# Optimization experiments

Measured on AMD Instinct MI355X. Metric: run time of the kernel, lower is better.

The kernel has to match this reference:

```python
import jax, jax.numpy as jnp
import numpy as np

EPS = 1e-05


def _project_to_poincare_ball(v, eps=EPS):
    # scale = clamp((1-eps)/(||v||+1e-10), max=1.0)
    norm = jnp.sqrt(jnp.sum(v * v, axis=-1, keepdims=True))
    scale = jnp.minimum((1.0 - eps) / (norm + 1e-10), 1.0)
    return v * scale


def setup_inputs() -> dict:
    key = jax.random.key(0)
    k1, k2 = jax.random.split(key)
    B, S, D, V = 2, 2048, 1024, 32000
    hidden_states = jax.random.normal(k1, (B, S, D), dtype=jnp.float32)
    weight = jax.random.normal(k2, (V, D), dtype=jnp.float32)
    return {"hidden_states": hidden_states, "weight": weight}


def reference(hidden_states, weight):
    eps = EPS
    B, S, D = hidden_states.shape
    x = _project_to_poincare_ball(hidden_states.reshape(-1, D), eps)  # (N, D)
    y = _project_to_poincare_ball(weight, eps)                        # (V, D)

    x_sq = jnp.sum(x * x, axis=-1)  # (N,)
    y_sq = jnp.sum(y * y, axis=-1)  # (V,)

    # NOTE: the original feeds this (non-squared) distance into the Poincare
    # formula (variable misnamed diff_norm_sq); we reproduce that exactly.
    d2 = x_sq[:, None] + y_sq[None, :] - 2.0 * jnp.einsum('nd,vd->nv', x, y)
    dist_euclid = jnp.sqrt(jnp.maximum(d2, 0.0))  # (N, V)

    denom = (1.0 - x_sq)[:, None] * (1.0 - y_sq)[None, :]  # (N, V)
    argument = 1.0 + 2.0 * dist_euclid / (denom + eps)
    argument = jnp.maximum(argument, 1.0 + eps)
    distances = jnp.arccosh(argument)  # (N, V)

    logits = -distances
    return logits.reshape(B, S, -1)
```

## Files before the change

kernel.cpp:

```cpp
#include <hip/hip_runtime.h>
#include <math.h>
#include <stdint.h>

#define EPS 1e-5f

typedef __bf16 bf16x8 __attribute__((ext_vector_type(8)));
typedef __bf16 bf16x4 __attribute__((ext_vector_type(4)));
typedef float  f32x4  __attribute__((ext_vector_type(4)));

constexpr int D  = 1024;
constexpr int BM = 128;
constexpr int BN = 128;

__global__ __launch_bounds__(256) void project_convert_kernel(
    const float* __restrict__ src, __bf16* __restrict__ dst,
    float* __restrict__ q_out)
{
    const int row = blockIdx.x;
    const int t = threadIdx.x;
    const float4 v = *(const float4*)(src + (size_t)row * D + t * 4);
    float s = v.x * v.x + v.y * v.y + v.z * v.z + v.w * v.w;
#pragma unroll
    for (int off = 32; off > 0; off >>= 1) s += __shfl_down(s, off);
    __shared__ float partial[4];
    __shared__ float s_scale;
    if ((t & 63) == 0) partial[t >> 6] = s;
    __syncthreads();
    if (t == 0) {
        float tot = partial[0] + partial[1] + partial[2] + partial[3];
        float norm = sqrtf(tot);
        float sc = fminf((1.0f - EPS) / (norm + 1e-10f), 1.0f);
        s_scale = sc;
        q_out[row] = sc * sc * tot;
    }
    __syncthreads();
    const float sc = s_scale;
    bf16x4 o = { (__bf16)(v.x * sc), (__bf16)(v.y * sc),
                 (__bf16)(v.z * sc), (__bf16)(v.w * sc) };
    *(bf16x4*)(dst + (size_t)row * D + t * 4) = o;
}

__device__ __forceinline__ void gload16(const void* g, void* l)
{
    __builtin_amdgcn_global_load_lds(
        (const __attribute__((address_space(1))) uint32_t*)g,
        (__attribute__((address_space(3))) uint32_t*)l, 16, 0, 0);
}

__global__ __launch_bounds__(256, 3) void hyp_gemm_bf16_kernel(
    const __bf16* __restrict__ Xb, const __bf16* __restrict__ Yb,
    const float* __restrict__ xq, const float* __restrict__ yq,
    float* __restrict__ out, int V, int nbx)
{
    constexpr int BK   = 64;
    constexpr int KT   = D / BK;
    constexpr int ROWB = BK * 2;

    __shared__ __bf16 As[BM * BK];
    __shared__ __bf16 Bs[BN * BK];

    const int wg = blockIdx.x;
    const int c = (gridDim.x & 7) ? wg : ((wg & 7) * (gridDim.x >> 3) + (wg >> 3));
    const int m0 = (c / nbx) * BM;
    const int n0 = (c % nbx) * BN;

    const int t = threadIdx.x;

    const int rt = t >> 3;
    const int gsrc = (t & 7) ^ (rt & 7);
    const char* xg = (const char*)(Xb + (size_t)(m0 + rt) * D) + gsrc * 16;
    const char* yg = (const char*)(Yb + (size_t)(n0 + rt) * D) + gsrc * 16;
    char* la = (char*)As + t * 16;
    char* lb = (char*)Bs + t * 16;

    const int lane = t & 63;
    const int ln   = lane & 15;
    const int quad = lane >> 4;
    const int wave = t >> 6;
    const int wm = (wave & 1) * 64;
    const int wn = (wave >> 1) * 64;
    const int swz = ln & 7;

    f32x4 acc[4][4] = {};

#pragma unroll
    for (int kt = 0; kt < KT; ++kt) {
        __syncthreads();
        const int ko = kt * 128;
#pragma unroll
        for (int j = 0; j < 4; ++j) {
            gload16(xg + j * 65536 + ko, la + j * 4096);
            gload16(yg + j * 65536 + ko, lb + j * 4096);
        }
        __syncthreads();
#pragma unroll
        for (int ks = 0; ks < 2; ++ks) {
            bf16x8 af[4], bfr[4];
#pragma unroll
            for (int i = 0; i < 4; ++i) {
                const int ga = ((ks * 4 + quad) ^ swz) * 16;
                af[i]  = *(const bf16x8*)((const char*)As + (wm + i * 16 + ln) * ROWB + ga);
                bfr[i] = *(const bf16x8*)((const char*)Bs + (wn + i * 16 + ln) * ROWB + ga);
            }
#pragma unroll
            for (int mt = 0; mt < 4; ++mt)
#pragma unroll
                for (int nt = 0; nt < 4; ++nt)
                    acc[mt][nt] = __builtin_amdgcn_mfma_f32_16x16x32_bf16(
                        af[mt], bfr[nt], acc[mt][nt], 0, 0, 0);
        }
    }

    float yqv[4], omy[4];
    int gcv[4];
#pragma unroll
    for (int nt = 0; nt < 4; ++nt) {
        const int gc = n0 + wn + nt * 16 + ln;
        gcv[nt] = gc;
        yqv[nt] = yq[gc];
        omy[nt] = 1.0f - yqv[nt];
    }
#pragma unroll
    for (int mt = 0; mt < 4; ++mt) {
#pragma unroll
        for (int r = 0; r < 4; ++r) {
            const int gm = m0 + wm + mt * 16 + quad * 4 + r;
            const float xqv = xq[gm];
            const float omx = 1.0f - xqv;
            float* orow = out + (size_t)gm * V;
#pragma unroll
            for (int nt = 0; nt < 4; ++nt) {
                const float dot = acc[mt][nt][r];
                float d2 = fmaxf(xqv + yqv[nt] - 2.0f * dot, 0.0f);
                float d  = __builtin_amdgcn_sqrtf(d2);
                float denom = omx * omy[nt] + EPS;
                float w = d * __builtin_amdgcn_rcpf(denom);
                float res;
                if (__builtin_expect(w >= 4.0f, 1)) {
                    res = __logf(2.0f + 4.0f * w);
                } else {
                    float arg = fmaxf(1.0f + 2.0f * w, 1.0f + EPS);
                    res = __logf(arg + __builtin_amdgcn_sqrtf(arg * arg - 1.0f));
                }
                orow[gcv[nt]] = -res;
            }
        }
    }
}

constexpr int LDT = 40;

__global__ __launch_bounds__(256) void row_stats_kernel(
    const float* __restrict__ src, float* __restrict__ scale_out,
    float* __restrict__ sq_out)
{
    const int row = blockIdx.x;
    const int t = threadIdx.x;
    const float4 v = *(const float4*)(src + (size_t)row * D + t * 4);
    float s = v.x * v.x + v.y * v.y + v.z * v.z + v.w * v.w;
#pragma unroll
    for (int off = 32; off > 0; off >>= 1) s += __shfl_down(s, off);
    __shared__ float partial[4];
    if ((t & 63) == 0) partial[t >> 6] = s;
    __syncthreads();
    if (t == 0) {
        float tot = partial[0] + partial[1] + partial[2] + partial[3];
        float norm = sqrtf(tot);
        float sc = fminf((1.0f - EPS) / (norm + 1e-10f), 1.0f);
        scale_out[row] = sc;
        sq_out[row] = sc * sc * tot;
    }
}

__global__ __launch_bounds__(256) void hyp_gemm_kernel(
    const float* __restrict__ X, const float* __restrict__ Y,
    const float* __restrict__ sx, const float* __restrict__ xq,
    const float* __restrict__ sy, const float* __restrict__ yq,
    float* __restrict__ out, int V)
{
    constexpr int BK = 32;
    __shared__ __bf16 As[BM * LDT];
    __shared__ __bf16 Bs[BN * LDT];

    const int t  = threadIdx.x;
    const int m0 = blockIdx.y * BM;
    const int n0 = blockIdx.x * BN;

    const int sr = t >> 3;
    const int scol = t & 7;

    const float* xg = X + (size_t)(m0 + sr) * D + scol * 4;
    const float* yg = Y + (size_t)(n0 + sr) * D + scol * 4;

    const int lane = t & 63;
    const int wave = t >> 6;
    const int wm = (wave & 1) * 64;
    const int wn = (wave >> 1) * 64;
    const int ln = lane & 15;
    const int quad = lane >> 4;

    f32x4 acc[4][4] = {};

    float4 pa[4], pb[4];
#pragma unroll
    for (int j = 0; j < 4; ++j) {
        pa[j] = *(const float4*)(xg + (size_t)j * 32 * D);
        pb[j] = *(const float4*)(yg + (size_t)j * 32 * D);
    }

    constexpr int KT = D / BK;
    for (int kt = 0; kt < KT; ++kt) {
        __syncthreads();
#pragma unroll
        for (int j = 0; j < 4; ++j) {
            bf16x4 a4 = { (__bf16)pa[j].x, (__bf16)pa[j].y, (__bf16)pa[j].z, (__bf16)pa[j].w };
            bf16x4 b4 = { (__bf16)pb[j].x, (__bf16)pb[j].y, (__bf16)pb[j].z, (__bf16)pb[j].w };
            *(bf16x4*)&As[(sr + 32 * j) * LDT + scol * 4] = a4;
            *(bf16x4*)&Bs[(sr + 32 * j) * LDT + scol * 4] = b4;
        }
        __syncthreads();
        if (kt + 1 < KT) {
            const int koff = (kt + 1) * BK;
#pragma unroll
            for (int j = 0; j < 4; ++j) {
                pa[j] = *(const float4*)(xg + (size_t)j * 32 * D + koff);
                pb[j] = *(const float4*)(yg + (size_t)j * 32 * D + koff);
            }
        }
        bf16x8 af[4], bfr[4];
#pragma unroll
        for (int i = 0; i < 4; ++i) {
            af[i]  = *(const bf16x8*)&As[(wm + i * 16 + ln) * LDT + quad * 8];
            bfr[i] = *(const bf16x8*)&Bs[(wn + i * 16 + ln) * LDT + quad * 8];
        }
#pragma unroll
        for (int mt = 0; mt < 4; ++mt)
#pragma unroll
            for (int nt = 0; nt < 4; ++nt)
                acc[mt][nt] = __builtin_amdgcn_mfma_f32_16x16x32_bf16(
                    af[mt], bfr[nt], acc[mt][nt], 0, 0, 0);
    }

    float yqv[4], syv[4];
    int gcv[4];
#pragma unroll
    for (int nt = 0; nt < 4; ++nt) {
        const int gc = n0 + wn + nt * 16 + ln;
        gcv[nt] = gc;
        yqv[nt] = yq[gc];
        syv[nt] = sy[gc];
    }
#pragma unroll
    for (int mt = 0; mt < 4; ++mt) {
#pragma unroll
        for (int r = 0; r < 4; ++r) {
            const int gm = m0 + wm + mt * 16 + quad * 4 + r;
            const float xqv = xq[gm];
            const float sxv = sx[gm];
            const float omx = 1.0f - xqv;
            float* orow = out + (size_t)gm * V;
#pragma unroll
            for (int nt = 0; nt < 4; ++nt) {
                const float raw = acc[mt][nt][r];
                const float dot = sxv * syv[nt] * raw;
                float d2 = xqv + yqv[nt] - 2.0f * dot;
                float dd = __builtin_amdgcn_sqrtf(fmaxf(d2, 0.0f));
                float denom = omx * (1.0f - yqv[nt]) + EPS;
                float arg = 1.0f + 2.0f * dd * __builtin_amdgcn_rcpf(denom);
                arg = fmaxf(arg, 1.0f + EPS);
                float res = -__logf(arg + __builtin_amdgcn_sqrtf(arg * arg - 1.0f));
                orow[gcv[nt]] = res;
            }
        }
    }
}

extern "C" void kernel_launch(void* const* d_in, const int* in_sizes, int n_in,
                              void* d_out, int out_size, void* d_ws, size_t ws_size,
                              hipStream_t stream)
{
    const float* X = (const float*)d_in[0];
    const float* Y = (const float*)d_in[1];
    float* out = (float*)d_out;

    const int N = in_sizes[0] / D;
    const int V = in_sizes[1] / D;

    const size_t need = (size_t)(N + V) * D * 2 + (size_t)(N + V) * 4;

    if (ws_size >= need && (N % BM) == 0 && (V % BN) == 0) {
        __bf16* Xb = (__bf16*)d_ws;
        __bf16* Yb = Xb + (size_t)N * D;
        float* xq = (float*)(Yb + (size_t)V * D);
        float* yq = xq + N;

        project_convert_kernel<<<N, 256, 0, stream>>>(X, Xb, xq);
        project_convert_kernel<<<V, 256, 0, stream>>>(Y, Yb, yq);

        const int nbx = V / BN;
        const int nwg = nbx * (N / BM);
        hyp_gemm_bf16_kernel<<<nwg, 256, 0, stream>>>(Xb, Yb, xq, yq, out, V, nbx);
    } else {
        float* sx = (float*)d_ws;
        float* xq = sx + N;
        float* sy = xq + N;
        float* yq = sy + V;

        row_stats_kernel<<<N, 256, 0, stream>>>(X, sx, xq);
        row_stats_kernel<<<V, 256, 0, stream>>>(Y, sy, yq);

        dim3 grid(V / BN, N / BM);
        hyp_gemm_kernel<<<grid, 256, 0, stream>>>(X, Y, sx, xq, sy, yq, out, V);
    }
}
```

Measured before the change: 898.5 us.

## Use 256x256 tiles with double-buffered LDS and 512-thread blocks

Result: no change. 909.2 us (+1.2%).

```diff
diff --git a/kernel.cpp b/kernel.cpp
--- a/kernel.cpp
+++ b/kernel.cpp
@@ -9,8 +9,6 @@
 typedef float  f32x4  __attribute__((ext_vector_type(4)));
 
 constexpr int D  = 1024;
-constexpr int BM = 128;
-constexpr int BN = 128;
 
 __global__ __launch_bounds__(256) void project_convert_kernel(
     const float* __restrict__ src, __bf16* __restrict__ dst,
@@ -47,22 +45,25 @@
         (__attribute__((address_space(3))) uint32_t*)l, 16, 0, 0);
 }
 
-__global__ __launch_bounds__(256, 3) void hyp_gemm_bf16_kernel(
+#define WAITVM(N) asm volatile("s_waitcnt vmcnt(" #N ")" ::: "memory")
+#define WAITLGKM0 asm volatile("s_waitcnt lgkmcnt(0)" ::: "memory")
+
+__global__ __launch_bounds__(512, 2) void hyp_gemm_256_kernel(
     const __bf16* __restrict__ Xb, const __bf16* __restrict__ Yb,
     const float* __restrict__ xq, const float* __restrict__ yq,
     float* __restrict__ out, int V, int nbx)
 {
-    constexpr int BK   = 64;
-    constexpr int KT   = D / BK;
-    constexpr int ROWB = BK * 2;
-
-    __shared__ __bf16 As[BM * BK];
-    __shared__ __bf16 Bs[BN * BK];
+    constexpr int BK = 64;
+    constexpr int KT = D / BK;
+    constexpr int BUFB = 256 * BK * 2;
+
+    __shared__ __bf16 As[2 * 256 * BK];
+    __shared__ __bf16 Bs[2 * 256 * BK];
 
     const int wg = blockIdx.x;
     const int c = (gridDim.x & 7) ? wg : ((wg & 7) * (gridDim.x >> 3) + (wg >> 3));
-    const int m0 = (c / nbx) * BM;
-    const int n0 = (c % nbx) * BN;
+    const int m0 = (c / nbx) * 256;
+    const int n0 = (c % nbx) * 256;
 
     const int t = threadIdx.x;
 
@@ -70,45 +71,69 @@
     const int gsrc = (t & 7) ^ (rt & 7);
     const char* xg = (const char*)(Xb + (size_t)(m0 + rt) * D) + gsrc * 16;
     const char* yg = (const char*)(Yb + (size_t)(n0 + rt) * D) + gsrc * 16;
-    char* la = (char*)As + t * 16;
-    char* lb = (char*)Bs + t * 16;
 
     const int lane = t & 63;
     const int ln   = lane & 15;
     const int quad = lane >> 4;
     const int wave = t >> 6;
-    const int wm = (wave & 1) * 64;
-    const int wn = (wave >> 1) * 64;
+    const int wm = (wave >> 2) * 128;
+    const int wn = (wave & 3) * 64;
     const int swz = ln & 7;
 
-    f32x4 acc[4][4] = {};
-
-#pragma unroll
-    for (int kt = 0; kt < KT; ++kt) {
-        __syncthreads();
+    f32x4 acc[8][4] = {};
+
+    auto STAGE = [&](int kt, int b) {
         const int ko = kt * 128;
 #pragma unroll
-        for (int j = 0; j < 4; ++j) {
-            gload16(xg + j * 65536 + ko, la + j * 4096);
-            gload16(yg + j * 65536 + ko, lb + j * 4096);
-        }
-        __syncthreads();
+        for (int j = 0; j < 4; ++j)
+            gload16(xg + j * 131072 + ko, (char*)As + b * BUFB + j * 8192 + t * 16);
+#pragma unroll
+        for (int j = 0; j < 4; ++j)
+            gload16(yg + j * 131072 + ko, (char*)Bs + b * BUFB + j * 8192 + t * 16);
+    };
+
+    auto COMPUTE = [&](int b) {
+        const char* Ab = (const char*)As + b * BUFB;
+        const char* Bb = (const char*)Bs + b * BUFB;
 #pragma unroll
         for (int ks = 0; ks < 2; ++ks) {
-            bf16x8 af[4], bfr[4];
-#pragma unroll
-            for (int i = 0; i < 4; ++i) {
-                const int ga = ((ks * 4 + quad) ^ swz) * 16;
-                af[i]  = *(const bf16x8*)((const char*)As + (wm + i * 16 + ln) * ROWB + ga);
-                bfr[i] = *(const bf16x8*)((const char*)Bs + (wn + i * 16 + ln) * ROWB + ga);
-            }
-#pragma unroll
-            for (int mt = 0; mt < 4; ++mt)
+            const int ga = ((ks * 4 + quad) ^ swz) * 16;
+            bf16x8 af[8], bfr[4];
+#pragma unroll
+            for (int i = 0; i < 8; ++i)
+                af[i] = *(const bf16x8*)(Ab + (wm + i * 16 + ln) * 128 + ga);
+#pragma unroll
+            for (int i = 0; i < 4; ++i)
+                bfr[i] = *(const bf16x8*)(Bb + (wn + i * 16 + ln) * 128 + ga);
+            __builtin_amdgcn_s_setprio(1);
+#pragma unroll
+            for (int mt = 0; mt < 8; ++mt)
 #pragma unroll
                 for (int nt = 0; nt < 4; ++nt)
                     acc[mt][nt] = __builtin_amdgcn_mfma_f32_16x16x32_bf16(
                         af[mt], bfr[nt], acc[mt][nt], 0, 0, 0);
-        }
+            __builtin_amdgcn_s_setprio(0);
+        }
+    };
+
+    STAGE(0, 0);
+#pragma unroll 2
+    for (int kt = 0; kt < KT; ++kt) {
+        const int b = kt & 1;
+        if (kt + 1 < KT) {
+            STAGE(kt + 1, b ^ 1);
+            WAITVM(8);
+        } else {
+            WAITVM(0);
+        }
+        __builtin_amdgcn_sched_barrier(0);
+        __builtin_amdgcn_s_barrier();
+        __builtin_amdgcn_sched_barrier(0);
+        COMPUTE(b);
+        WAITLGKM0;
+        __builtin_amdgcn_sched_barrier(0);
+        __builtin_amdgcn_s_barrier();
+        __builtin_amdgcn_sched_barrier(0);
     }
 
     float yqv[4], omy[4];
@@ -121,7 +146,7 @@
         omy[nt] = 1.0f - yqv[nt];
     }
 #pragma unroll
-    for (int mt = 0; mt < 4; ++mt) {
+    for (int mt = 0; mt < 8; ++mt) {
 #pragma unroll
         for (int r = 0; r < 4; ++r) {
             const int gm = m0 + wm + mt * 16 + quad * 4 + r;
@@ -148,6 +173,7 @@
     }
 }
 
+constexpr int FBM = 128, FBN = 128;
 constexpr int LDT = 40;
 
 __global__ __launch_bounds__(256) void row_stats_kernel(
@@ -179,12 +205,12 @@
     float* __restrict__ out, int V)
 {
     constexpr int BK = 32;
-    __shared__ __bf16 As[BM * LDT];
-    __shared__ __bf16 Bs[BN * LDT];
+    __shared__ __bf16 As[FBM * LDT];
+    __shared__ __bf16 Bs[FBN * LDT];
 
     const int t  = threadIdx.x;
-    const int m0 = blockIdx.y * BM;
-    const int n0 = blockIdx.x * BN;
+    const int m0 = blockIdx.y * FBM;
+    const int n0 = blockIdx.x * FBN;
 
     const int sr = t >> 3;
     const int scol = t & 7;
@@ -288,7 +314,7 @@
 
     const size_t need = (size_t)(N + V) * D * 2 + (size_t)(N + V) * 4;
 
-    if (ws_size >= need && (N % BM) == 0 && (V % BN) == 0) {
+    if (ws_size >= need && (N % 256) == 0 && (V % 256) == 0) {
         __bf16* Xb = (__bf16*)d_ws;
         __bf16* Yb = Xb + (size_t)N * D;
         float* xq = (float*)(Yb + (size_t)V * D);
@@ -297,9 +323,9 @@
         project_convert_kernel<<<N, 256, 0, stream>>>(X, Xb, xq);
         project_convert_kernel<<<V, 256, 0, stream>>>(Y, Yb, yq);
 
-        const int nbx = V / BN;
-        const int nwg = nbx * (N / BM);
-        hyp_gemm_bf16_kernel<<<nwg, 256, 0, stream>>>(Xb, Yb, xq, yq, out, V, nbx);
+        const int nbx = V / 256;
+        const int nwg = nbx * (N / 256);
+        hyp_gemm_256_kernel<<<nwg, 512, 0, stream>>>(Xb, Yb, xq, yq, out, V, nbx);
     } else {
         float* sx = (float*)d_ws;
         float* xq = sx + N;
@@ -309,7 +335,7 @@
         row_stats_kernel<<<N, 256, 0, stream>>>(X, sx, xq);
         row_stats_kernel<<<V, 256, 0, stream>>>(Y, sy, yq);
 
-        dim3 grid(V / BN, N / BM);
+        dim3 grid(V / FBN, N / FBM);
         hyp_gemm_kernel<<<grid, 256, 0, stream>>>(X, Y, sx, xq, sy, yq, out, V);
     }
 }
```
